# Kernel optimization log

Hardware: AMD Instinct MI355X
Metric: run time of the kernel (lower is better)

The kernel has to match this reference:

```python
import jax, jax.numpy as jnp
import numpy as np
import math

B, C, H, L, E = 4, 4, 8, 512, 128  # L == win_size + 1


def setup_inputs() -> dict:
    key = jax.random.key(0)
    kq, kk, kv, ks = jax.random.split(key, 4)
    queries = jax.random.normal(kq, (B, C, H, L, E), jnp.float32)
    keys = jax.random.normal(kk, (B, C, H, L, E), jnp.float32)
    values = jax.random.normal(kv, (B, C, H, L, E), jnp.float32)
    sigma = jax.random.normal(ks, (B, C, H, L), jnp.float32)
    # triangular causal mask: True above the diagonal (masked out)
    tri = jnp.triu(jnp.ones((L, L), dtype=bool), k=1)
    attn_mask = jnp.broadcast_to(tri[None, None, None], (B, 1, 1, L, L))
    return {"queries": queries, "keys": keys, "values": values,
            "sigma": sigma, "attn_mask": attn_mask}


def reference(queries, keys, values, sigma, attn_mask):
    Bq, Cq, Hq, Lq, Eq = queries.shape
    scale = 1.0 / math.sqrt(Eq)
    # scores: [B,C,H,L,L]
    scores = jnp.einsum("bchle,bchme->bchlm", queries, keys)
    scores = jnp.where(attn_mask, -jnp.inf, scores)
    attn = scale * scores

    # Gaussian prior from learned sigma
    sig = jax.nn.sigmoid(sigma * 5.0) + 1e-5
    sig = jnp.power(3.0, sig) - 1.0            # [B,C,H,L]
    sig = sig[..., None]                        # [B,C,H,L,1]
    idx = jnp.arange(Lq, dtype=queries.dtype)
    dist = jnp.abs(idx[:, None] - idx[None, :])  # [L,L]
    inv_norm = 1.0 / (math.sqrt(2.0 * math.pi) * sig)
    prior = inv_norm * jnp.exp(-(dist ** 2) / (2.0 * sig ** 2))  # [B,C,H,L,L]

    series = jax.nn.softmax(attn, axis=-1)      # dropout p=0.0 -> identity
    V = jnp.einsum("bchlm,bchme->bchle", series, values)
    sigma_out = jnp.broadcast_to(sig, prior.shape)
    return V, series, prior, sigma_out
```

## Files before the change

kernel.cpp:

```cpp
#include <hip/hip_runtime.h>
#include <math.h>

#define L 512
#define E 128
#define NT 8

typedef __attribute__((ext_vector_type(8))) short bf16x8;
typedef __attribute__((ext_vector_type(4))) float f32x4;
typedef __attribute__((ext_vector_type(4))) unsigned short u16x4;

__device__ __forceinline__ unsigned short bf16_rne(float x) {
  unsigned u = __builtin_bit_cast(unsigned, x);
  unsigned r = u + 0x7FFFu + ((u >> 16) & 1u);
  return (unsigned short)(r >> 16);
}
__device__ __forceinline__ float bf16_to_f(unsigned short h) {
  unsigned u = ((unsigned)h) << 16;
  return __builtin_bit_cast(float, u);
}

__global__ __launch_bounds__(256) void prior_kernel(
    const float* __restrict__ sigma,
    float* __restrict__ prior,
    float* __restrict__ sigma_out) {
  const int half = threadIdx.x >> 7;
  const int t128 = threadIdx.x & 127;
  const int m0 = t128 * 4;
#pragma unroll 4
  for (int i = 0; i < 16; ++i) {
    const int row = blockIdx.x * 32 + i * 2 + half;
    const int l = row & (L - 1);
    const float x = sigma[row];
    const float sg = 1.0f / (1.0f + __expf(-5.0f * x)) + 1e-5f;
    const float sigp = expm1f(sg * 1.0986122886681098f);
    const float inv_norm = 0.3989422804014327f / sigp;
    const float c = -1.0f / (2.0f * sigp * sigp);

    f32x4 pr, so;
    so[0] = so[1] = so[2] = so[3] = sigp;
#pragma unroll
    for (int j = 0; j < 4; ++j) {
      float d = (float)(l - (m0 + j));
      pr[j] = inv_norm * __expf(c * d * d);
    }
    const size_t off = (size_t)row * L + m0;
    __builtin_nontemporal_store(pr, (f32x4*)(prior + off));
    __builtin_nontemporal_store(so, (f32x4*)(sigma_out + off));
  }
}

__global__ __launch_bounds__(256, 2) void attn_kernel(
    const float* __restrict__ Q,
    const float* __restrict__ K,
    const float* __restrict__ V,
    float* __restrict__ outV,
    float* __restrict__ series) {
  const int bch = blockIdx.x;
  const int tid = threadIdx.x;
  const int w = tid >> 6, lane = tid & 63, r = lane & 15, g = lane >> 4;

  __shared__ char smem[34816];
  char* sKhi = smem;
  char* sKlo = smem + 17408;
  char* sP = smem;
  char* sVt = smem + 9216;

  const size_t base = (size_t)bch * (L * E);
  const float scale = 0.08838834764831845f;

#pragma unroll 1
  for (int pass = 0; pass < 2; ++pass) {
    const int qt = pass ? 7 - blockIdx.y : blockIdx.y;
    const int qbase = qt * 64;
    __syncthreads();

    bf16x8 qh[4], ql[4];
    {
      const float* qrow = Q + base + (size_t)(qbase + 16 * w + r) * E;
#pragma unroll
      for (int ks = 0; ks < 4; ++ks) {
        const int e0 = 32 * ks + 8 * g;
        f32x4 a = *(const f32x4*)(qrow + e0);
        f32x4 b = *(const f32x4*)(qrow + e0 + 4);
#pragma unroll
        for (int j = 0; j < 4; ++j) {
          float xa = a[j] * scale;
          unsigned short ha = bf16_rne(xa);
          qh[ks][j] = (short)ha;
          ql[ks][j] = (short)bf16_rne(xa - bf16_to_f(ha));
          float xb = b[j] * scale;
          unsigned short hb = bf16_rne(xb);
          qh[ks][4 + j] = (short)hb;
          ql[ks][4 + j] = (short)bf16_rne(xb - bf16_to_f(hb));
        }
      }
    }

    f32x4 Sacc[NT][4];
#pragma unroll
    for (int t = 0; t < NT; ++t)
#pragma unroll
      for (int cb = 0; cb < 4; ++cb) Sacc[t][cb] = (f32x4){0.f, 0.f, 0.f, 0.f};

#pragma unroll
    for (int t = 0; t < NT; ++t) {
      if (t <= qt) {
        __syncthreads();
#pragma unroll
        for (int i = 0; i < 8; ++i) {
          int f = i * 256 + tid;
          int row = f >> 5;
          int e0 = (f & 31) * 4;
          f32x4 kv =
              *(const f32x4*)(K + base + (size_t)(t * 64 + row) * E + e0);
          u16x4 h4, l4;
#pragma unroll
          for (int j = 0; j < 4; ++j) {
            unsigned short h = bf16_rne(kv[j]);
            h4[j] = h;
            l4[j] = bf16_rne(kv[j] - bf16_to_f(h));
          }
          *(u16x4*)(sKhi + row * 272 + e0 * 2) = h4;
          *(u16x4*)(sKlo + row * 272 + e0 * 2) = l4;
        }
        __syncthreads();

#pragma unroll
        for (int ks = 0; ks < 4; ++ks) {
#pragma unroll
          for (int cb = 0; cb < 4; ++cb) {
            const int kb = (16 * cb + r) * 272 + (32 * ks + 8 * g) * 2;
            bf16x8 bh = *(const bf16x8*)(sKhi + kb);
            bf16x8 bl = *(const bf16x8*)(sKlo + kb);
            f32x4 acc = Sacc[t][cb];
            acc = __builtin_amdgcn_mfma_f32_16x16x32_bf16(qh[ks], bh, acc, 0, 0, 0);
            acc = __builtin_amdgcn_mfma_f32_16x16x32_bf16(ql[ks], bh, acc, 0, 0, 0);
            acc = __builtin_amdgcn_mfma_f32_16x16x32_bf16(qh[ks], bl, acc, 0, 0, 0);
            Sacc[t][cb] = acc;
          }
        }
      }
    }

    float mrow[4], srow[4], inv[4];
#pragma unroll
    for (int reg = 0; reg < 4; ++reg) mrow[reg] = -__builtin_inff();

#pragma unroll
    for (int t = 0; t < NT; ++t) {
      if (t > qt) continue;
#pragma unroll
      for (int cb = 0; cb < 4; ++cb)
#pragma unroll
        for (int reg = 0; reg < 4; ++reg) {
          float s = Sacc[t][cb][reg];
          if (t == qt && (16 * cb + r) > (16 * w + 4 * g + reg))
            s = -__builtin_inff();
          Sacc[t][cb][reg] = s;
          mrow[reg] = fmaxf(mrow[reg], s);
        }
    }
#pragma unroll
    for (int off = 1; off <= 8; off <<= 1)
#pragma unroll
      for (int reg = 0; reg < 4; ++reg)
        mrow[reg] = fmaxf(mrow[reg], __shfl_xor(mrow[reg], off, 64));

#pragma unroll
    for (int reg = 0; reg < 4; ++reg) srow[reg] = 0.0f;
#pragma unroll
    for (int t = 0; t < NT; ++t) {
      if (t > qt) continue;
#pragma unroll
      for (int cb = 0; cb < 4; ++cb)
#pragma unroll
        for (int reg = 0; reg < 4; ++reg) {
          float p = __expf(Sacc[t][cb][reg] - mrow[reg]);
          Sacc[t][cb][reg] = p;
          srow[reg] += p;
        }
    }
#pragma unroll
    for (int off = 1; off <= 8; off <<= 1)
#pragma unroll
      for (int reg = 0; reg < 4; ++reg)
        srow[reg] += __shfl_xor(srow[reg], off, 64);
#pragma unroll
    for (int reg = 0; reg < 4; ++reg) inv[reg] = 1.0f / srow[reg];

    f32x4 Oacc[8];
#pragma unroll
    for (int cb = 0; cb < 8; ++cb) Oacc[cb] = (f32x4){0.f, 0.f, 0.f, 0.f};

#pragma unroll
    for (int t = 0; t < NT; ++t) {
      if (t <= qt) {
        __syncthreads();
#pragma unroll
        for (int cb = 0; cb < 4; ++cb)
#pragma unroll
          for (int reg = 0; reg < 4; ++reg) {
            float p = Sacc[t][cb][reg] * inv[reg];
            *(unsigned short*)(sP + (16 * w + 4 * g + reg) * 144 +
                               (16 * cb + r) * 2) = bf16_rne(p);
          }
#pragma unroll
        for (int bb = 0; bb < 2; ++bb) {
          int bidx = tid + 256 * bb;
          int m0 = (bidx >> 5) * 4;
          int e0 = (bidx & 31) * 4;
          const float* vrow = V + base + (size_t)(t * 64 + m0) * E + e0;
          f32x4 R0 = *(const f32x4*)(vrow);
          f32x4 R1 = *(const f32x4*)(vrow + E);
          f32x4 R2 = *(const f32x4*)(vrow + 2 * E);
          f32x4 R3 = *(const f32x4*)(vrow + 3 * E);
#pragma unroll
          for (int i = 0; i < 4; ++i) {
            u16x4 wv;
            wv[0] = bf16_rne(R0[i]);
            wv[1] = bf16_rne(R1[i]);
            wv[2] = bf16_rne(R2[i]);
            wv[3] = bf16_rne(R3[i]);
            int e = e0 + i;
            int byte = e * 144 + m0 * 2;
            byte ^= ((e >> 2) & 7) << 4;
            *(u16x4*)(sVt + byte) = wv;
          }
        }
        __syncthreads();

#pragma unroll
        for (int cb = 0; cb < 4; ++cb)
#pragma unroll
          for (int reg = 0; reg < 4; ++reg) {
            size_t off = ((size_t)bch * L + qbase + 16 * w + 4 * g + reg) * L +
                         t * 64 + 16 * cb + r;
            __builtin_nontemporal_store(Sacc[t][cb][reg] * inv[reg],
                                        series + off);
          }

#pragma unroll
        for (int ks = 0; ks < 2; ++ks) {
          bf16x8 ap = *(const bf16x8*)(sP + (16 * w + r) * 144 +
                                       (32 * ks + 8 * g) * 2);
#pragma unroll
          for (int cb = 0; cb < 8; ++cb) {
            int e = 16 * cb + r;
            int byte = e * 144 + (32 * ks + 8 * g) * 2;
            byte ^= ((e >> 2) & 7) << 4;
            bf16x8 bv = *(const bf16x8*)(sVt + byte);
            Oacc[cb] = __builtin_amdgcn_mfma_f32_16x16x32_bf16(ap, bv, Oacc[cb],
                                                               0, 0, 0);
          }
        }
      } else {
#pragma unroll
        for (int cb = 0; cb < 4; ++cb)
#pragma unroll
          for (int reg = 0; reg < 4; ++reg) {
            size_t off = ((size_t)bch * L + qbase + 16 * w + 4 * g + reg) * L +
                         t * 64 + 16 * cb + r;
            __builtin_nontemporal_store(0.0f, series + off);
          }
      }
    }

#pragma unroll
    for (int cb = 0; cb < 8; ++cb)
#pragma unroll
      for (int reg = 0; reg < 4; ++reg)
        outV[base + (size_t)(qbase + 16 * w + 4 * g + reg) * E + 16 * cb + r] =
            Oacc[cb][reg];
  }
}

extern "C" void kernel_launch(void* const* d_in, const int* in_sizes, int n_in,
                              void* d_out, int out_size, void* d_ws,
                              size_t ws_size, hipStream_t stream) {
  const float* Q = (const float*)d_in[0];
  const float* K = (const float*)d_in[1];
  const float* V = (const float*)d_in[2];
  const float* sigma = (const float*)d_in[3];

  float* out = (float*)d_out;
  float* outV = out;
  float* series = out + 8388608;
  float* prior = out + 41943040;
  float* sigma_out = out + 75497472;

  attn_kernel<<<dim3(128, 4), 256, 0, stream>>>(Q, K, V, outV, series);
  prior_kernel<<<dim3(2048), 256, 0, stream>>>(sigma, prior, sigma_out);
}
```

Before: 643.7 us.

## Fuse QK and PV into one pass with unnormalized exp and deferred scaling

```diff
diff --git a/kernel.cpp b/kernel.cpp
--- a/kernel.cpp
+++ b/kernel.cpp
@@ -56,222 +56,161 @@
     float* __restrict__ outV,
     float* __restrict__ series) {
   const int bch = blockIdx.x;
+  const int qt = 7 - blockIdx.y;
   const int tid = threadIdx.x;
   const int w = tid >> 6, lane = tid & 63, r = lane & 15, g = lane >> 4;
 
-  __shared__ char smem[34816];
-  char* sKhi = smem;
-  char* sKlo = smem + 17408;
-  char* sP = smem;
-  char* sVt = smem + 9216;
+  __shared__ char smem[47104];
+  char* sK = smem;
+  char* sVt = smem + 17408;
+  char* sP = smem + 37888;
 
   const size_t base = (size_t)bch * (L * E);
+  const int qbase = qt * 64;
   const float scale = 0.08838834764831845f;
 
-#pragma unroll 1
-  for (int pass = 0; pass < 2; ++pass) {
-    const int qt = pass ? 7 - blockIdx.y : blockIdx.y;
-    const int qbase = qt * 64;
-    __syncthreads();
-
-    bf16x8 qh[4], ql[4];
-    {
-      const float* qrow = Q + base + (size_t)(qbase + 16 * w + r) * E;
+  bf16x8 qh[4], ql[4];
+  {
+    const float* qrow = Q + base + (size_t)(qbase + 16 * w + r) * E;
+#pragma unroll
+    for (int ks = 0; ks < 4; ++ks) {
+      const int e0 = 32 * ks + 8 * g;
+      f32x4 a = *(const f32x4*)(qrow + e0);
+      f32x4 b = *(const f32x4*)(qrow + e0 + 4);
+#pragma unroll
+      for (int j = 0; j < 4; ++j) {
+        float xa = a[j] * scale;
+        unsigned short ha = bf16_rne(xa);
+        qh[ks][j] = (short)ha;
+        ql[ks][j] = (short)bf16_rne(xa - bf16_to_f(ha));
+        float xb = b[j] * scale;
+        unsigned short hb = bf16_rne(xb);
+        qh[ks][4 + j] = (short)hb;
+        ql[ks][4 + j] = (short)bf16_rne(xb - bf16_to_f(hb));
+      }
+    }
+  }
+
+  f32x4 Sacc[NT][4];
+  float srow[4] = {0.f, 0.f, 0.f, 0.f};
+  f32x4 Oacc[8];
+#pragma unroll
+  for (int cb = 0; cb < 8; ++cb) Oacc[cb] = (f32x4){0.f, 0.f, 0.f, 0.f};
+
+#pragma unroll
+  for (int t = 0; t < NT; ++t) {
+    if (t <= qt) {
+      __syncthreads();
+#pragma unroll
+      for (int i = 0; i < 8; ++i) {
+        int f = i * 256 + tid;
+        int row = f >> 5;
+        int e0 = (f & 31) * 4;
+        f32x4 kv = *(const f32x4*)(K + base + (size_t)(t * 64 + row) * E + e0);
+        u16x4 h4;
+#pragma unroll
+        for (int j = 0; j < 4; ++j) h4[j] = bf16_rne(kv[j]);
+        *(u16x4*)(sK + row * 272 + e0 * 2) = h4;
+      }
+#pragma unroll
+      for (int bb = 0; bb < 2; ++bb) {
+        int bidx = tid + 256 * bb;
+        int m0 = (bidx >> 5) * 4;
+        int e0 = (bidx & 31) * 4;
+        const float* vrow = V + base + (size_t)(t * 64 + m0) * E + e0;
+        f32x4 R0 = *(const f32x4*)(vrow);
+        f32x4 R1 = *(const f32x4*)(vrow + E);
+        f32x4 R2 = *(const f32x4*)(vrow + 2 * E);
+        f32x4 R3 = *(const f32x4*)(vrow + 3 * E);
+#pragma unroll
+        for (int i = 0; i < 4; ++i) {
+          u16x4 wv;
+          wv[0] = bf16_rne(R0[i]);
+          wv[1] = bf16_rne(R1[i]);
+          wv[2] = bf16_rne(R2[i]);
+          wv[3] = bf16_rne(R3[i]);
+          int e = e0 + i;
+          int byte = e * 160 + m0 * 2;
+          byte ^= ((e >> 2) & 7) << 4;
+          *(u16x4*)(sVt + byte) = wv;
+        }
+      }
+      __syncthreads();
+
+#pragma unroll
+      for (int cb = 0; cb < 4; ++cb) Sacc[t][cb] = (f32x4){0.f, 0.f, 0.f, 0.f};
 #pragma unroll
       for (int ks = 0; ks < 4; ++ks) {
-        const int e0 = 32 * ks + 8 * g;
-        f32x4 a = *(const f32x4*)(qrow + e0);
-        f32x4 b = *(const f32x4*)(qrow + e0 + 4);
-#pragma unroll
-        for (int j = 0; j < 4; ++j) {
-          float xa = a[j] * scale;
-          unsigned short ha = bf16_rne(xa);
-          qh[ks][j] = (short)ha;
-          ql[ks][j] = (short)bf16_rne(xa - bf16_to_f(ha));
-          float xb = b[j] * scale;
-          unsigned short hb = bf16_rne(xb);
-          qh[ks][4 + j] = (short)hb;
-          ql[ks][4 + j] = (short)bf16_rne(xb - bf16_to_f(hb));
-        }
-      }
-    }
-
-    f32x4 Sacc[NT][4];
-#pragma unroll
-    for (int t = 0; t < NT; ++t)
-#pragma unroll
-      for (int cb = 0; cb < 4; ++cb) Sacc[t][cb] = (f32x4){0.f, 0.f, 0.f, 0.f};
-
-#pragma unroll
-    for (int t = 0; t < NT; ++t) {
-      if (t <= qt) {
-        __syncthreads();
-#pragma unroll
-        for (int i = 0; i < 8; ++i) {
-          int f = i * 256 + tid;
-          int row = f >> 5;
-          int e0 = (f & 31) * 4;
-          f32x4 kv =
-              *(const f32x4*)(K + base + (size_t)(t * 64 + row) * E + e0);
-          u16x4 h4, l4;
-#pragma unroll
-          for (int j = 0; j < 4; ++j) {
-            unsigned short h = bf16_rne(kv[j]);
-            h4[j] = h;
-            l4[j] = bf16_rne(kv[j] - bf16_to_f(h));
-          }
-          *(u16x4*)(sKhi + row * 272 + e0 * 2) = h4;
-          *(u16x4*)(sKlo + row * 272 + e0 * 2) = l4;
-        }
-        __syncthreads();
-
-#pragma unroll
-        for (int ks = 0; ks < 4; ++ks) {
-#pragma unroll
-          for (int cb = 0; cb < 4; ++cb) {
-            const int kb = (16 * cb + r) * 272 + (32 * ks + 8 * g) * 2;
-            bf16x8 bh = *(const bf16x8*)(sKhi + kb);
-            bf16x8 bl = *(const bf16x8*)(sKlo + kb);
-            f32x4 acc = Sacc[t][cb];
-            acc = __builtin_amdgcn_mfma_f32_16x16x32_bf16(qh[ks], bh, acc, 0, 0, 0);
-            acc = __builtin_amdgcn_mfma_f32_16x16x32_bf16(ql[ks], bh, acc, 0, 0, 0);
-            acc = __builtin_amdgcn_mfma_f32_16x16x32_bf16(qh[ks], bl, acc, 0, 0, 0);
-            Sacc[t][cb] = acc;
-          }
-        }
-      }
-    }
-
-    float mrow[4], srow[4], inv[4];
-#pragma unroll
-    for (int reg = 0; reg < 4; ++reg) mrow[reg] = -__builtin_inff();
-
-#pragma unroll
-    for (int t = 0; t < NT; ++t) {
-      if (t > qt) continue;
+#pragma unroll
+        for (int cb = 0; cb < 4; ++cb) {
+          const int kb = (16 * cb + r) * 272 + (32 * ks + 8 * g) * 2;
+          bf16x8 bh = *(const bf16x8*)(sK + kb);
+          f32x4 acc = Sacc[t][cb];
+          acc = __builtin_amdgcn_mfma_f32_16x16x32_bf16(qh[ks], bh, acc, 0, 0, 0);
+          acc = __builtin_amdgcn_mfma_f32_16x16x32_bf16(ql[ks], bh, acc, 0, 0, 0);
+          Sacc[t][cb] = acc;
+        }
+      }
+
 #pragma unroll
       for (int cb = 0; cb < 4; ++cb)
 #pragma unroll
         for (int reg = 0; reg < 4; ++reg) {
-          float s = Sacc[t][cb][reg];
-          if (t == qt && (16 * cb + r) > (16 * w + 4 * g + reg))
-            s = -__builtin_inff();
-          Sacc[t][cb][reg] = s;
-          mrow[reg] = fmaxf(mrow[reg], s);
-        }
-    }
-#pragma unroll
-    for (int off = 1; off <= 8; off <<= 1)
-#pragma unroll
-      for (int reg = 0; reg < 4; ++reg)
-        mrow[reg] = fmaxf(mrow[reg], __shfl_xor(mrow[reg], off, 64));
-
-#pragma unroll
-    for (int reg = 0; reg < 4; ++reg) srow[reg] = 0.0f;
-#pragma unroll
-    for (int t = 0; t < NT; ++t) {
-      if (t > qt) continue;
-#pragma unroll
-      for (int cb = 0; cb < 4; ++cb)
-#pragma unroll
-        for (int reg = 0; reg < 4; ++reg) {
-          float p = __expf(Sacc[t][cb][reg] - mrow[reg]);
+          float p = __expf(Sacc[t][cb][reg]);
+          if (t == qt && (16 * cb + r) > (16 * w + 4 * g + reg)) p = 0.f;
           Sacc[t][cb][reg] = p;
           srow[reg] += p;
-        }
+          *(unsigned short*)(sP + (16 * w + 4 * g + reg) * 144 +
+                             (16 * cb + r) * 2) = bf16_rne(p);
+        }
+      asm volatile("s_waitcnt lgkmcnt(0)" ::: "memory");
+      __builtin_amdgcn_sched_barrier(0);
+
+#pragma unroll
+      for (int ks = 0; ks < 2; ++ks) {
+        bf16x8 ap =
+            *(const bf16x8*)(sP + (16 * w + r) * 144 + (32 * ks + 8 * g) * 2);
+#pragma unroll
+        for (int cb = 0; cb < 8; ++cb) {
+          int e = 16 * cb + r;
+          int byte = e * 160 + (32 * ks + 8 * g) * 2;
+          byte ^= ((e >> 2) & 7) << 4;
+          bf16x8 bv = *(const bf16x8*)(sVt + byte);
+          Oacc[cb] = __builtin_amdgcn_mfma_f32_16x16x32_bf16(ap, bv, Oacc[cb],
+                                                             0, 0, 0);
+        }
+      }
     }
-#pragma unroll
-    for (int off = 1; off <= 8; off <<= 1)
-#pragma unroll
-      for (int reg = 0; reg < 4; ++reg)
-        srow[reg] += __shfl_xor(srow[reg], off, 64);
-#pragma unroll
-    for (int reg = 0; reg < 4; ++reg) inv[reg] = 1.0f / srow[reg];
-
-    f32x4 Oacc[8];
-#pragma unroll
-    for (int cb = 0; cb < 8; ++cb) Oacc[cb] = (f32x4){0.f, 0.f, 0.f, 0.f};
-
-#pragma unroll
-    for (int t = 0; t < NT; ++t) {
-      if (t <= qt) {
-        __syncthreads();
-#pragma unroll
-        for (int cb = 0; cb < 4; ++cb)
-#pragma unroll
-          for (int reg = 0; reg < 4; ++reg) {
-            float p = Sacc[t][cb][reg] * inv[reg];
-            *(unsigned short*)(sP + (16 * w + 4 * g + reg) * 144 +
-                               (16 * cb + r) * 2) = bf16_rne(p);
-          }
-#pragma unroll
-        for (int bb = 0; bb < 2; ++bb) {
-          int bidx = tid + 256 * bb;
-          int m0 = (bidx >> 5) * 4;
-          int e0 = (bidx & 31) * 4;
-          const float* vrow = V + base + (size_t)(t * 64 + m0) * E + e0;
-          f32x4 R0 = *(const f32x4*)(vrow);
-          f32x4 R1 = *(const f32x4*)(vrow + E);
-          f32x4 R2 = *(const f32x4*)(vrow + 2 * E);
-          f32x4 R3 = *(const f32x4*)(vrow + 3 * E);
-#pragma unroll
-          for (int i = 0; i < 4; ++i) {
-            u16x4 wv;
-            wv[0] = bf16_rne(R0[i]);
-            wv[1] = bf16_rne(R1[i]);
-            wv[2] = bf16_rne(R2[i]);
-            wv[3] = bf16_rne(R3[i]);
-            int e = e0 + i;
-            int byte = e * 144 + m0 * 2;
-            byte ^= ((e >> 2) & 7) << 4;
-            *(u16x4*)(sVt + byte) = wv;
-          }
-        }
-        __syncthreads();
-
-#pragma unroll
-        for (int cb = 0; cb < 4; ++cb)
-#pragma unroll
-          for (int reg = 0; reg < 4; ++reg) {
-            size_t off = ((size_t)bch * L + qbase + 16 * w + 4 * g + reg) * L +
-                         t * 64 + 16 * cb + r;
-            __builtin_nontemporal_store(Sacc[t][cb][reg] * inv[reg],
-                                        series + off);
-          }
-
-#pragma unroll
-        for (int ks = 0; ks < 2; ++ks) {
-          bf16x8 ap = *(const bf16x8*)(sP + (16 * w + r) * 144 +
-                                       (32 * ks + 8 * g) * 2);
-#pragma unroll
-          for (int cb = 0; cb < 8; ++cb) {
-            int e = 16 * cb + r;
-            int byte = e * 144 + (32 * ks + 8 * g) * 2;
-            byte ^= ((e >> 2) & 7) << 4;
-            bf16x8 bv = *(const bf16x8*)(sVt + byte);
-            Oacc[cb] = __builtin_amdgcn_mfma_f32_16x16x32_bf16(ap, bv, Oacc[cb],
-                                                               0, 0, 0);
-          }
-        }
-      } else {
-#pragma unroll
-        for (int cb = 0; cb < 4; ++cb)
-#pragma unroll
-          for (int reg = 0; reg < 4; ++reg) {
-            size_t off = ((size_t)bch * L + qbase + 16 * w + 4 * g + reg) * L +
-                         t * 64 + 16 * cb + r;
-            __builtin_nontemporal_store(0.0f, series + off);
-          }
-      }
-    }
-
-#pragma unroll
-    for (int cb = 0; cb < 8; ++cb)
-#pragma unroll
-      for (int reg = 0; reg < 4; ++reg)
-        outV[base + (size_t)(qbase + 16 * w + 4 * g + reg) * E + 16 * cb + r] =
-            Oacc[cb][reg];
-  }
+  }
+
+  float inv[4];
+#pragma unroll
+  for (int off = 1; off <= 8; off <<= 1)
+#pragma unroll
+    for (int reg = 0; reg < 4; ++reg)
+      srow[reg] += __shfl_xor(srow[reg], off, 64);
+#pragma unroll
+  for (int reg = 0; reg < 4; ++reg) inv[reg] = 1.0f / srow[reg];
+
+#pragma unroll
+  for (int t = 0; t < NT; ++t) {
+#pragma unroll
+    for (int cb = 0; cb < 4; ++cb)
+#pragma unroll
+      for (int reg = 0; reg < 4; ++reg) {
+        size_t off = ((size_t)bch * L + qbase + 16 * w + 4 * g + reg) * L +
+                     t * 64 + 16 * cb + r;
+        float val = (t <= qt) ? Sacc[t][cb][reg] * inv[reg] : 0.f;
+        __builtin_nontemporal_store(val, series + off);
+      }
+  }
+
+#pragma unroll
+  for (int cb = 0; cb < 8; ++cb)
+#pragma unroll
+    for (int reg = 0; reg < 4; ++reg)
+      outV[base + (size_t)(qbase + 16 * w + 4 * g + reg) * E + 16 * cb + r] =
+          Oacc[cb][reg] * inv[reg];
 }
 
 extern "C" void kernel_launch(void* const* d_in, const int* in_sizes, int n_in,
@@ -288,6 +227,6 @@
   float* prior = out + 41943040;
   float* sigma_out = out + 75497472;
 
-  attn_kernel<<<dim3(128, 4), 256, 0, stream>>>(Q, K, V, outV, series);
+  attn_kernel<<<dim3(128, 8), 256, 0, stream>>>(Q, K, V, outV, series);
   prior_kernel<<<dim3(2048), 256, 0, stream>>>(sigma, prior, sigma_out);
 }
```

Result: faster. 526.6 us (-18.2%).
